# Kernel optimization log

Measured on AMD Instinct MI355X. Metric: run time of the kernel, lower is better.

Reference implementation:

```python
import jax, jax.numpy as jnp
import numpy as np

# ---- constants matching the original module's globals ----
H = 16          # self.h: number of bit levels; self.n = h per the source
TP = 8          # self.tp: parallel coordinate channels
N_K = 2         # random masks per flipped bit
T = 512         # T_train: tokens per block
N_TRNBR = 128   # neighbor count
K_VOCAB = 128   # sampled vocab count
N_VOCAB = 50257 # full vocab size V for sampled softmax correction
D = 256         # embedding dim
RATIO_COS = 1.0
RATIO_CRO = 0.1
C_CNC = 2 * H * N_K + 1  # candidate locations per token = 65


def setup_inputs() -> dict:
    key = jax.random.key(0)
    ks = jax.random.split(key, 8)
    n = H  # code: self.n = h
    sta_loc = jax.random.randint(ks[0], (T, TP), 1 - n, n, dtype=jnp.int32)
    nei_loc = jax.random.randint(ks[1], (T, N_TRNBR, TP), 1 - n, n, dtype=jnp.int32)
    voc_loc = jax.random.randint(ks[2], (T, K_VOCAB, TP), 1 - n, n, dtype=jnp.int32)
    sta_emb = jax.random.normal(ks[3], (T, D), dtype=jnp.float32)
    nei_emb = jax.random.normal(ks[4], (T, N_TRNBR, D), dtype=jnp.float32)
    voc_emb = jax.random.normal(ks[5], (T, K_VOCAB, D), dtype=jnp.float32)
    # raw random numbers for generate_random_masks: randint(0, self.n)
    rand_masks = jax.random.randint(ks[6], (T, H, N_K, TP), 0, n, dtype=jnp.int32)
    # converge mode: mask is all ones (generate_mask with converge=True)
    mask = jnp.ones((T, N_TRNBR), dtype=bool)
    return {"sta_loc": sta_loc, "nei_loc": nei_loc, "voc_loc": voc_loc,
            "sta_emb": sta_emb, "nei_emb": nei_emb, "voc_emb": voc_emb,
            "rand_masks": rand_masks, "mask": mask}


def _cos_similarity(c1, c2):
    # sign product: (+1 if >=0 else -1) for each operand
    sg = ((2 * (c1 >= 0).astype(jnp.int32) - 1) *
          (2 * (c2 >= 0).astype(jnp.int32) - 1)).astype(jnp.float32)
    x = ((jnp.abs(c1) ^ jnp.abs(c2)) + 1).astype(jnp.float32)
    # torch.frexp exponent of v>=1 equals floor(log2(v)) + 1
    expo = jnp.floor(jnp.log2(x)) + 1.0
    return sg * (1.0 - expo / H)


def _connection(sta_loc, rand_masks):
    bits = jnp.arange(H, dtype=jnp.int32)
    flip_masks = (1 << bits)                          # [H]
    flipped = sta_loc[:, None, :] ^ flip_masks[None, :, None]  # [T,H,TP]
    # note operator precedence in source: rn & (2**i - 1)
    rm = rand_masks & (flip_masks - 1)[None, :, None, None]    # [T,H,N_K,TP]
    res = (flipped[:, :, None, :] ^ rm).reshape(sta_loc.shape[0], H * N_K, TP)
    return jnp.concatenate([res, sta_loc[:, None, :], -res], axis=1)  # [T,C,TP]


def _normalize(x):
    return x / jnp.maximum(jnp.linalg.norm(x, axis=-1, keepdims=True), 1e-12)


def reference(sta_loc, nei_loc, voc_loc, sta_emb, nei_emb, voc_emb, rand_masks, mask):
    cnc_loc = _connection(sta_loc, rand_masks)          # [T, C, TP]
    lth = mask.sum(axis=1).astype(jnp.float32) + 1e-12  # [T]

    # euclidean-space cosine targets: [T, N_trnbr]
    eu_cos_val = jnp.einsum('td,tnd->tn', _normalize(sta_emb), _normalize(nei_emb))
    # use_eu_norm == True branch: ||sta|| * ||voc|| -> [T, K_vocab]
    eu_cro_nrm = (jnp.linalg.norm(sta_emb, axis=-1, keepdims=True) *
                  jnp.linalg.norm(voc_emb, axis=-1))

    pos_loc = jnp.concatenate([nei_loc, voc_loc], axis=1)           # [T, P, TP]
    cos_sta_pos = _cos_similarity(sta_loc[:, None, :], pos_loc)     # [T, P, TP]
    cos_sta_pos_sum = cos_sta_pos.sum(axis=-1)                      # [T, P]
    cos_cnc_pos = _cos_similarity(cnc_loc[:, None, :, :], pos_loc[:, :, None, :])  # [T,P,C,TP]
    ct_val = (cos_sta_pos_sum[:, :, None, None]
              - cos_sta_pos[:, :, None, :] + cos_cnc_pos) / TP      # [T,P,C,TP]

    # cosine-matching loss over neighbors
    eu = eu_cos_val[:, :, None, None]                               # [T,N,1,1]
    loss_cos = ((ct_val[:, :N_TRNBR] - eu) ** 2 * jnp.abs(eu)
                * mask[:, :, None, None].astype(jnp.float32))
    loss_cos = loss_cos.sum(axis=1) / lth[:, None, None]            # [T, C, TP]

    # sampled softmax CE (uniform proposal), positive class at vocab index 0
    z = ct_val[:, N_TRNBR:] * eu_cro_nrm[:, :, None, None]          # [T, K, C, TP]
    corr = jnp.where(jnp.arange(K_VOCAB) == 0, 0.0,
                     jnp.log(N_VOCAB / K_VOCAB)).astype(jnp.float32)
    zc = z + corr[None, :, None, None]
    loss_cro = jax.scipy.special.logsumexp(zc, axis=1) - zc[:, 0]   # [T, C, TP]

    loss_tot = RATIO_COS * loss_cos + RATIO_CRO * loss_cro

    # get_best_loc with cur_portion=1.0, cur_tp=tp -> pure argmin selection
    idx = jnp.argmin(loss_tot, axis=1)                              # [T, TP]
    gather = lambda a: jnp.take_along_axis(a, idx[:, None, :], axis=1)[:, 0]
    selected_locs = gather(cnc_loc)                                 # [T, TP]
    real_loss_cos = gather(loss_cos).mean(axis=-1)                  # [T]
    real_loss_cro = gather(loss_cro).mean(axis=-1)
    real_loss_tot = gather(loss_tot).mean(axis=-1)
    return selected_locs, real_loss_cos, real_loss_cro, real_loss_tot
```

## Files before the change

### kernel.cpp

```cpp
#include <hip/hip_runtime.h>
#include <math.h>

#define T_DIM 512
#define TP 8
#define H 16
#define N_K 2
#define N_TRNBR 128
#define K_VOCAB 128
#define D_DIM 256
#define C_CNC 65
#define NPOS 256
#define BLOCK 576

__device__ __forceinline__ float cos_sim(int c1, int c2) {
    float sg = ((c1 >= 0) == (c2 >= 0)) ? 1.0f : -1.0f;
    int a1 = c1 < 0 ? -c1 : c1;
    int a2 = c2 < 0 ? -c2 : c2;
    int x = (a1 ^ a2) + 1;
    int expo = 32 - __clz(x);
    return sg * (1.0f - (float)expo * 0.0625f);
}

__global__ __launch_bounds__(BLOCK) void critigraph_kernel(
    const int* __restrict__ sta_loc,
    const int* __restrict__ nei_loc,
    const int* __restrict__ voc_loc,
    const float* __restrict__ sta_emb,
    const float* __restrict__ nei_emb,
    const float* __restrict__ voc_emb,
    const int* __restrict__ rand_masks,
    float* __restrict__ out)
{
    const int t = blockIdx.x;
    const int tid = threadIdx.x;

    __shared__ int   s_sta[TP];
    __shared__ int   s_rand[H * N_K * TP];
    __shared__ int   s_pos[NPOS * TP];
    __shared__ float s_csp[NPOS * TP];
    __shared__ float s_css[NPOS];
    __shared__ float s_eu[128];
    __shared__ float s_nrm[128];
    __shared__ float s_dot[128], s_nn[128], s_vv[128];
    __shared__ float s_ss;
    __shared__ float s_lcos[C_CNC * TP], s_lcro[C_CNC * TP], s_ltot[C_CNC * TP];
    __shared__ int   s_cnc[C_CNC * TP];
    __shared__ float s_sel[3 * TP];

    if (tid < TP) s_sta[tid] = sta_loc[t * TP + tid];
    if (tid < H * N_K * TP) s_rand[tid] = rand_masks[t * H * N_K * TP + tid];

    if (tid < 512) {
        const int g = tid >> 2, sub = tid & 3;
        const float4* sp = reinterpret_cast<const float4*>(sta_emb + (size_t)t * D_DIM);
        const float4* np_ = reinterpret_cast<const float4*>(nei_emb + ((size_t)t * 128 + g) * D_DIM);
        const float4* vp = reinterpret_cast<const float4*>(voc_emb + ((size_t)t * 128 + g) * D_DIM);
        float sd = 0.f, nn = 0.f, vv = 0.f, ss = 0.f;
        #pragma unroll
        for (int i = 0; i < 16; ++i) {
            const int i4 = sub + 4 * i;
            float4 a = sp[i4];
            float4 b = np_[i4];
            float4 c = vp[i4];
            sd += a.x * b.x + a.y * b.y + a.z * b.z + a.w * b.w;
            nn += b.x * b.x + b.y * b.y + b.z * b.z + b.w * b.w;
            vv += c.x * c.x + c.y * c.y + c.z * c.z + c.w * c.w;
            ss += a.x * a.x + a.y * a.y + a.z * a.z + a.w * a.w;
        }
        sd += __shfl_xor(sd, 1); sd += __shfl_xor(sd, 2);
        nn += __shfl_xor(nn, 1); nn += __shfl_xor(nn, 2);
        vv += __shfl_xor(vv, 1); vv += __shfl_xor(vv, 2);
        ss += __shfl_xor(ss, 1); ss += __shfl_xor(ss, 2);
        if (sub == 0) {
            s_dot[g] = sd; s_nn[g] = nn; s_vv[g] = vv;
            if (g == 0) s_ss = ss;
        }
    }
    __syncthreads();

    if (tid < 128) {
        const float ns = sqrtf(s_ss);
        const float cs = fmaxf(ns, 1e-12f);
        const float cn = fmaxf(sqrtf(s_nn[tid]), 1e-12f);
        s_eu[tid] = s_dot[tid] / (cn * cs);
        s_nrm[tid] = ns * sqrtf(s_vv[tid]);
    }

    for (int item = tid; item < NPOS * TP; item += BLOCK) {
        const int j = item >> 3, p = item & 7;
        const int pl = (j < 128) ? nei_loc[((size_t)t * 128 + j) * TP + p]
                                 : voc_loc[((size_t)t * 128 + (j - 128)) * TP + p];
        s_pos[j * TP + p] = pl;
        s_csp[j * TP + p] = cos_sim(s_sta[p], pl);
    }
    __syncthreads();

    if (tid < NPOS) {
        float s = 0.f;
        #pragma unroll
        for (int p = 0; p < TP; ++p) s += s_csp[tid * TP + p];
        s_css[tid] = s;
    }
    __syncthreads();

    if (tid < C_CNC * TP) {
        const int c = tid >> 3, p = tid & 7;
        const int sta = s_sta[p];
        int v;
        if (c == 32) {
            v = sta;
        } else {
            const int cc = (c < 32) ? c : (c - 33);
            const int h = cc >> 1, k = cc & 1;
            const int r = (sta ^ (1 << h)) ^ (s_rand[(h * N_K + k) * TP + p] & ((1 << h) - 1));
            v = (c < 32) ? r : -r;
        }

        float lc = 0.f;
        for (int j = 0; j < 128; ++j) {
            const float ct = (s_css[j] - s_csp[j * TP + p] + cos_sim(v, s_pos[j * TP + p])) * 0.125f;
            const float e = s_eu[j];
            const float d = ct - e;
            lc += d * d * fabsf(e);
        }
        lc *= (1.0f / 128.0f);

        const float CORR = logf(50257.0f / 128.0f);
        float m = -INFINITY, ssum = 0.f, z0 = 0.f;
        for (int k = 0; k < 128; ++k) {
            const int j = 128 + k;
            const float ct = (s_css[j] - s_csp[j * TP + p] + cos_sim(v, s_pos[j * TP + p])) * 0.125f;
            const float z = ct * s_nrm[k] + ((k == 0) ? 0.0f : CORR);
            if (k == 0) z0 = z;
            const float nm = fmaxf(m, z);
            ssum = ssum * expf(m - nm) + expf(z - nm);
            m = nm;
        }
        const float lcro = m + logf(ssum) - z0;

        s_lcos[c * TP + p] = lc;
        s_lcro[c * TP + p] = lcro;
        s_ltot[c * TP + p] = lc + 0.1f * lcro;
        s_cnc[c * TP + p] = v;
    }
    __syncthreads();

    if (tid < TP) {
        const int p = tid;
        float best = s_ltot[p];
        int bi = 0;
        for (int c = 1; c < C_CNC; ++c) {
            const float vv = s_ltot[c * TP + p];
            if (vv < best) { best = vv; bi = c; }
        }
        out[t * TP + p] = (float)s_cnc[bi * TP + p];
        s_sel[p] = s_lcos[bi * TP + p];
        s_sel[TP + p] = s_lcro[bi * TP + p];
        s_sel[2 * TP + p] = s_ltot[bi * TP + p];
    }
    __syncthreads();

    if (tid == 0) {
        float a = 0.f, b = 0.f, c = 0.f;
        #pragma unroll
        for (int p = 0; p < TP; ++p) {
            a += s_sel[p]; b += s_sel[TP + p]; c += s_sel[2 * TP + p];
        }
        out[T_DIM * TP + t] = a * (1.0f / TP);
        out[T_DIM * TP + T_DIM + t] = b * (1.0f / TP);
        out[T_DIM * TP + 2 * T_DIM + t] = c * (1.0f / TP);
    }
}

extern "C" void kernel_launch(void* const* d_in, const int* in_sizes, int n_in,
                              void* d_out, int out_size, void* d_ws, size_t ws_size,
                              hipStream_t stream) {
    const int* sta_loc = (const int*)d_in[0];
    const int* nei_loc = (const int*)d_in[1];
    const int* voc_loc = (const int*)d_in[2];
    const float* sta_emb = (const float*)d_in[3];
    const float* nei_emb = (const float*)d_in[4];
    const float* voc_emb = (const float*)d_in[5];
    const int* rand_masks = (const int*)d_in[6];
    float* out = (float*)d_out;

    critigraph_kernel<<<T_DIM, BLOCK, 0, stream>>>(
        sta_loc, nei_loc, voc_loc, sta_emb, nei_emb, voc_emb, rand_masks, out);
}
```

Measured before the change: 218.3 us.

## Split per-token work across neighbor/vocab blocks and add finalize kernel

The single fused kernel becomes two. The main kernel uses a 2D grid, so one block handles the neighbor (cosine) side and another the vocab (cross-entropy) side. Each writes per-candidate losses to workspace, and a small second kernel does the argmin and the averaging. It also adds a bit-trick cosine similarity, precomputed per-position partial sums, exp2-based online softmax with a select-only rescale, and wave-parallel handling of the 65th candidate. This removes the serial dependency where each thread did both 128-length loops, and raises parallelism. The cost is a second launch and a round trip of the losses through global memory.

```diff
diff --git a/kernel.cpp b/kernel.cpp
--- a/kernel.cpp
+++ b/kernel.cpp
@@ -3,25 +3,24 @@
 
 #define T_DIM 512
 #define TP 8
-#define H 16
-#define N_K 2
-#define N_TRNBR 128
-#define K_VOCAB 128
-#define D_DIM 256
-#define C_CNC 65
-#define NPOS 256
-#define BLOCK 576
-
-__device__ __forceinline__ float cos_sim(int c1, int c2) {
-    float sg = ((c1 >= 0) == (c2 >= 0)) ? 1.0f : -1.0f;
-    int a1 = c1 < 0 ? -c1 : c1;
-    int a2 = c2 < 0 ? -c2 : c2;
-    int x = (a1 ^ a2) + 1;
-    int expo = 32 - __clz(x);
-    return sg * (1.0f - (float)expo * 0.0625f);
-}
-
-__global__ __launch_bounds__(BLOCK) void critigraph_kernel(
+#define NC 65
+#define NJ 128
+#define LOG2E 1.4426950408889634f
+#define LN2   0.6931471805599453f
+
+__device__ __forceinline__ float csim(int va, int vs, int qmix) {
+    const int sgn = (vs ^ qmix) & 0x80000000;
+    const int x = va ^ (qmix & 0x7fffffff);
+    const float u0 = fmaf((float)__clz(x + 1), 0.0625f, -1.0f);
+    return __int_as_float(__float_as_int(u0) ^ sgn);
+}
+
+__device__ __forceinline__ int make_v(int c, int sta, int rnd_cc_h , int h) {
+    const int r = (sta ^ (1 << h)) ^ (rnd_cc_h & ((1 << h) - 1));
+    return r;
+}
+
+__global__ __launch_bounds__(512, 8) void cg_main(
     const int* __restrict__ sta_loc,
     const int* __restrict__ nei_loc,
     const int* __restrict__ voc_loc,
@@ -29,146 +28,217 @@
     const float* __restrict__ nei_emb,
     const float* __restrict__ voc_emb,
     const int* __restrict__ rand_masks,
+    float* __restrict__ wcos,
+    float* __restrict__ wcro)
+{
+    const int t = blockIdx.x;
+    const int side = blockIdx.y;
+    const int tid = threadIdx.x;
+
+    __shared__ int2  s_pc[NJ * TP];
+    __shared__ float s_w[NJ];
+    __shared__ float s_css[NJ];
+    __shared__ float s_dot[NJ], s_nn[NJ];
+    __shared__ float s_ss;
+    __shared__ int   s_sta[TP];
+    __shared__ int   s_rand[256];
+
+    if (tid < TP) s_sta[tid] = sta_loc[t * TP + tid];
+    if (tid < 256) s_rand[tid] = rand_masks[t * 256 + tid];
+
+    {
+        const float* emb = (side == 0) ? nei_emb : voc_emb;
+        const int g = tid >> 2, sub = tid & 3;
+        const float4* ep = (const float4*)(emb + ((size_t)t * NJ + g) * 256);
+        const float4* sp = (const float4*)(sta_emb + (size_t)t * 256);
+        float dd = 0.f, nn = 0.f, ss = 0.f;
+        #pragma unroll
+        for (int i = 0; i < 16; ++i) {
+            const int i4 = sub + 4 * i;
+            const float4 a = sp[i4];
+            const float4 b = ep[i4];
+            dd += a.x * b.x + a.y * b.y + a.z * b.z + a.w * b.w;
+            nn += b.x * b.x + b.y * b.y + b.z * b.z + b.w * b.w;
+            if (g == 0) ss += a.x * a.x + a.y * a.y + a.z * a.z + a.w * a.w;
+        }
+        dd += __shfl_xor(dd, 1); dd += __shfl_xor(dd, 2);
+        nn += __shfl_xor(nn, 1); nn += __shfl_xor(nn, 2);
+        if (g == 0) { ss += __shfl_xor(ss, 1); ss += __shfl_xor(ss, 2); }
+        if (sub == 0) { s_dot[g] = dd; s_nn[g] = nn; if (g == 0) s_ss = ss; }
+    }
+    __syncthreads();
+
+    {
+        const int* loc = (side == 0) ? nei_loc : voc_loc;
+        #pragma unroll
+        for (int item = tid; item < NJ * TP; item += 512) {
+            const int p = item & 7;
+            const int pl = loc[(size_t)t * (NJ * TP) + item];
+            const int qm = (pl < 0 ? -pl : pl) | (pl & 0x80000000);
+            const int sta = s_sta[p];
+            const float csp = csim(sta < 0 ? -sta : sta, sta & 0x80000000, qm);
+            s_pc[item].x = qm;
+            s_pc[item].y = __float_as_int(csp);
+        }
+    }
+    __syncthreads();
+
+    if (tid < NJ) {
+        float cs = 0.f;
+        #pragma unroll
+        for (int p = 0; p < TP; ++p) cs += __int_as_float(s_pc[tid * TP + p].y);
+        s_css[tid] = cs;
+        const float ns = sqrtf(s_ss);
+        if (side == 0) {
+            s_w[tid] = s_dot[tid] / (fmaxf(sqrtf(s_nn[tid]), 1e-12f) * fmaxf(ns, 1e-12f));
+        } else {
+            s_w[tid] = ns * sqrtf(s_nn[tid]) * (0.125f * LOG2E);
+        }
+    }
+    __syncthreads();
+
+    {
+        const float corrl2 = logf(50257.0f / 128.0f) * LOG2E;
+        #pragma unroll
+        for (int item = tid; item < NJ * TP; item += 512) {
+            const int j = item >> 3;
+            const float csp = __int_as_float(s_pc[item].y);
+            const float b = s_css[j] - csp;
+            float val;
+            if (side == 0) val = b;
+            else val = fmaf(b, s_w[j], (j == 0) ? 0.0f : corrl2);
+            s_pc[item].y = __float_as_int(val);
+        }
+    }
+    __syncthreads();
+
+    {
+        const int c = tid >> 3, p = tid & 7;
+        const int sta = s_sta[p];
+        int v;
+        if (c == 32) v = sta;
+        else {
+            const int cc = (c < 32) ? c : (c - 33);
+            const int h = cc >> 1;
+            const int r = make_v(c, sta, s_rand[cc * TP + p], h);
+            v = (c < 32) ? r : -r;
+        }
+        const int va = v < 0 ? -v : v;
+        const int vs = v & 0x80000000;
+
+        if (side == 0) {
+            float lc = 0.f;
+            #pragma unroll 4
+            for (int j = 0; j < NJ; ++j) {
+                const int2 pc = s_pc[j * TP + p];
+                const float u = csim(va, vs, pc.x);
+                const float e = s_w[j];
+                const float d = fmaf(__int_as_float(pc.y) + u, 0.125f, -e);
+                lc = fmaf(d * d, fabsf(e), lc);
+            }
+            wcos[((size_t)t * NC + c) * TP + p] = lc * 0.0078125f;
+        } else {
+            const int2 pc0 = s_pc[p];
+            const float u0 = csim(va, vs, pc0.x);
+            const float z0 = fmaf(u0, s_w[0], __int_as_float(pc0.y));
+            float m = z0, s = 1.0f;
+            #pragma unroll 4
+            for (int k = 1; k < NJ; ++k) {
+                const int2 pc = s_pc[k * TP + p];
+                const float u = csim(va, vs, pc.x);
+                const float z = fmaf(u, s_w[k], __int_as_float(pc.y));
+                const float nm = fmaxf(m, z);
+                const float e = exp2f(fminf(z, m) - nm);
+                const bool gt = z > m;
+                s = fmaf(s, gt ? e : 1.0f, gt ? 1.0f : e);
+                m = nm;
+            }
+            wcro[((size_t)t * NC + c) * TP + p] = (m - z0 + log2f(s)) * LN2;
+        }
+    }
+
+    {
+        const int p = tid >> 6;
+        const int lane = tid & 63;
+        const int sta = s_sta[p];
+        const int v = -((sta ^ (1 << 15)) ^ (s_rand[31 * TP + p] & 0x7fff));
+        const int va = v < 0 ? -v : v;
+        const int vs = v & 0x80000000;
+
+        if (side == 0) {
+            float lc = 0.f;
+            #pragma unroll
+            for (int jj = 0; jj < 2; ++jj) {
+                const int j = 2 * lane + jj;
+                const int2 pc = s_pc[j * TP + p];
+                const float u = csim(va, vs, pc.x);
+                const float e = s_w[j];
+                const float d = fmaf(__int_as_float(pc.y) + u, 0.125f, -e);
+                lc = fmaf(d * d, fabsf(e), lc);
+            }
+            #pragma unroll
+            for (int off = 1; off < 64; off <<= 1) lc += __shfl_xor(lc, off);
+            if (lane == 0) wcos[((size_t)t * NC + 64) * TP + p] = lc * 0.0078125f;
+        } else {
+            const int ka = 2 * lane, kb = 2 * lane + 1;
+            const int2 pa = s_pc[ka * TP + p];
+            const int2 pb = s_pc[kb * TP + p];
+            const float za = fmaf(csim(va, vs, pa.x), s_w[ka], __int_as_float(pa.y));
+            const float zb = fmaf(csim(va, vs, pb.x), s_w[kb], __int_as_float(pb.y));
+            float m = fmaxf(za, zb);
+            float s = exp2f(za - m) + exp2f(zb - m);
+            const float z0 = za;
+            #pragma unroll
+            for (int off = 1; off < 64; off <<= 1) {
+                const float om = __shfl_xor(m, off);
+                const float os = __shfl_xor(s, off);
+                const float nm = fmaxf(m, om);
+                s = fmaf(s, exp2f(m - nm), os * exp2f(om - nm));
+                m = nm;
+            }
+            if (lane == 0) wcro[((size_t)t * NC + 64) * TP + p] = (m - z0 + log2f(s)) * LN2;
+        }
+    }
+}
+
+__global__ __launch_bounds__(64) void cg_fin(
+    const int* __restrict__ sta_loc, const int* __restrict__ rand_masks,
+    const float* __restrict__ wcos, const float* __restrict__ wcro,
     float* __restrict__ out)
 {
     const int t = blockIdx.x;
     const int tid = threadIdx.x;
-
-    __shared__ int   s_sta[TP];
-    __shared__ int   s_rand[H * N_K * TP];
-    __shared__ int   s_pos[NPOS * TP];
-    __shared__ float s_csp[NPOS * TP];
-    __shared__ float s_css[NPOS];
-    __shared__ float s_eu[128];
-    __shared__ float s_nrm[128];
-    __shared__ float s_dot[128], s_nn[128], s_vv[128];
-    __shared__ float s_ss;
-    __shared__ float s_lcos[C_CNC * TP], s_lcro[C_CNC * TP], s_ltot[C_CNC * TP];
-    __shared__ int   s_cnc[C_CNC * TP];
-    __shared__ float s_sel[3 * TP];
-
-    if (tid < TP) s_sta[tid] = sta_loc[t * TP + tid];
-    if (tid < H * N_K * TP) s_rand[tid] = rand_masks[t * H * N_K * TP + tid];
-
-    if (tid < 512) {
-        const int g = tid >> 2, sub = tid & 3;
-        const float4* sp = reinterpret_cast<const float4*>(sta_emb + (size_t)t * D_DIM);
-        const float4* np_ = reinterpret_cast<const float4*>(nei_emb + ((size_t)t * 128 + g) * D_DIM);
-        const float4* vp = reinterpret_cast<const float4*>(voc_emb + ((size_t)t * 128 + g) * D_DIM);
-        float sd = 0.f, nn = 0.f, vv = 0.f, ss = 0.f;
-        #pragma unroll
-        for (int i = 0; i < 16; ++i) {
-            const int i4 = sub + 4 * i;
-            float4 a = sp[i4];
-            float4 b = np_[i4];
-            float4 c = vp[i4];
-            sd += a.x * b.x + a.y * b.y + a.z * b.z + a.w * b.w;
-            nn += b.x * b.x + b.y * b.y + b.z * b.z + b.w * b.w;
-            vv += c.x * c.x + c.y * c.y + c.z * c.z + c.w * c.w;
-            ss += a.x * a.x + a.y * a.y + a.z * a.z + a.w * a.w;
-        }
-        sd += __shfl_xor(sd, 1); sd += __shfl_xor(sd, 2);
-        nn += __shfl_xor(nn, 1); nn += __shfl_xor(nn, 2);
-        vv += __shfl_xor(vv, 1); vv += __shfl_xor(vv, 2);
-        ss += __shfl_xor(ss, 1); ss += __shfl_xor(ss, 2);
-        if (sub == 0) {
-            s_dot[g] = sd; s_nn[g] = nn; s_vv[g] = vv;
-            if (g == 0) s_ss = ss;
-        }
-    }
-    __syncthreads();
-
-    if (tid < 128) {
-        const float ns = sqrtf(s_ss);
-        const float cs = fmaxf(ns, 1e-12f);
-        const float cn = fmaxf(sqrtf(s_nn[tid]), 1e-12f);
-        s_eu[tid] = s_dot[tid] / (cn * cs);
-        s_nrm[tid] = ns * sqrtf(s_vv[tid]);
-    }
-
-    for (int item = tid; item < NPOS * TP; item += BLOCK) {
-        const int j = item >> 3, p = item & 7;
-        const int pl = (j < 128) ? nei_loc[((size_t)t * 128 + j) * TP + p]
-                                 : voc_loc[((size_t)t * 128 + (j - 128)) * TP + p];
-        s_pos[j * TP + p] = pl;
-        s_csp[j * TP + p] = cos_sim(s_sta[p], pl);
-    }
-    __syncthreads();
-
-    if (tid < NPOS) {
-        float s = 0.f;
-        #pragma unroll
-        for (int p = 0; p < TP; ++p) s += s_csp[tid * TP + p];
-        s_css[tid] = s;
-    }
-    __syncthreads();
-
-    if (tid < C_CNC * TP) {
-        const int c = tid >> 3, p = tid & 7;
-        const int sta = s_sta[p];
+    float sc = 0.f, sr = 0.f, st = 0.f;
+    if (tid < TP) {
+        const float* pc = wcos + (size_t)t * NC * TP + tid;
+        const float* pr = wcro + (size_t)t * NC * TP + tid;
+        float best = INFINITY, blc = 0.f, blr = 0.f;
+        int bc = 0;
+        for (int c = 0; c < NC; ++c) {
+            const float lc = pc[c * TP];
+            const float lr = pr[c * TP];
+            const float lt = fmaf(0.1f, lr, lc);
+            if (lt < best) { best = lt; bc = c; blc = lc; blr = lr; }
+        }
+        const int sta = sta_loc[t * TP + tid];
         int v;
-        if (c == 32) {
-            v = sta;
-        } else {
-            const int cc = (c < 32) ? c : (c - 33);
-            const int h = cc >> 1, k = cc & 1;
-            const int r = (sta ^ (1 << h)) ^ (s_rand[(h * N_K + k) * TP + p] & ((1 << h) - 1));
-            v = (c < 32) ? r : -r;
-        }
-
-        float lc = 0.f;
-        for (int j = 0; j < 128; ++j) {
-            const float ct = (s_css[j] - s_csp[j * TP + p] + cos_sim(v, s_pos[j * TP + p])) * 0.125f;
-            const float e = s_eu[j];
-            const float d = ct - e;
-            lc += d * d * fabsf(e);
-        }
-        lc *= (1.0f / 128.0f);
-
-        const float CORR = logf(50257.0f / 128.0f);
-        float m = -INFINITY, ssum = 0.f, z0 = 0.f;
-        for (int k = 0; k < 128; ++k) {
-            const int j = 128 + k;
-            const float ct = (s_css[j] - s_csp[j * TP + p] + cos_sim(v, s_pos[j * TP + p])) * 0.125f;
-            const float z = ct * s_nrm[k] + ((k == 0) ? 0.0f : CORR);
-            if (k == 0) z0 = z;
-            const float nm = fmaxf(m, z);
-            ssum = ssum * expf(m - nm) + expf(z - nm);
-            m = nm;
-        }
-        const float lcro = m + logf(ssum) - z0;
-
-        s_lcos[c * TP + p] = lc;
-        s_lcro[c * TP + p] = lcro;
-        s_ltot[c * TP + p] = lc + 0.1f * lcro;
-        s_cnc[c * TP + p] = v;
-    }
-    __syncthreads();
-
-    if (tid < TP) {
-        const int p = tid;
-        float best = s_ltot[p];
-        int bi = 0;
-        for (int c = 1; c < C_CNC; ++c) {
-            const float vv = s_ltot[c * TP + p];
-            if (vv < best) { best = vv; bi = c; }
-        }
-        out[t * TP + p] = (float)s_cnc[bi * TP + p];
-        s_sel[p] = s_lcos[bi * TP + p];
-        s_sel[TP + p] = s_lcro[bi * TP + p];
-        s_sel[2 * TP + p] = s_ltot[bi * TP + p];
-    }
-    __syncthreads();
-
+        if (bc == 32) v = sta;
+        else {
+            const int cc = (bc < 32) ? bc : (bc - 33);
+            const int h = cc >> 1;
+            const int r = (sta ^ (1 << h)) ^ (rand_masks[t * 256 + cc * TP + tid] & ((1 << h) - 1));
+            v = (bc < 32) ? r : -r;
+        }
+        out[t * TP + tid] = (float)v;
+        sc = blc; sr = blr; st = best;
+    }
+    sc += __shfl_xor(sc, 1); sc += __shfl_xor(sc, 2); sc += __shfl_xor(sc, 4);
+    sr += __shfl_xor(sr, 1); sr += __shfl_xor(sr, 2); sr += __shfl_xor(sr, 4);
+    st += __shfl_xor(st, 1); st += __shfl_xor(st, 2); st += __shfl_xor(st, 4);
     if (tid == 0) {
-        float a = 0.f, b = 0.f, c = 0.f;
-        #pragma unroll
-        for (int p = 0; p < TP; ++p) {
-            a += s_sel[p]; b += s_sel[TP + p]; c += s_sel[2 * TP + p];
-        }
-        out[T_DIM * TP + t] = a * (1.0f / TP);
-        out[T_DIM * TP + T_DIM + t] = b * (1.0f / TP);
-        out[T_DIM * TP + 2 * T_DIM + t] = c * (1.0f / TP);
+        out[T_DIM * TP + t] = sc * 0.125f;
+        out[T_DIM * TP + T_DIM + t] = sr * 0.125f;
+        out[T_DIM * TP + 2 * T_DIM + t] = st * 0.125f;
     }
 }
 
@@ -184,6 +254,10 @@
     const int* rand_masks = (const int*)d_in[6];
     float* out = (float*)d_out;
 
-    critigraph_kernel<<<T_DIM, BLOCK, 0, stream>>>(
-        sta_loc, nei_loc, voc_loc, sta_emb, nei_emb, voc_emb, rand_masks, out);
-}
+    float* wcos = (float*)d_ws;
+    float* wcro = wcos + (size_t)T_DIM * NC * TP;
+
+    cg_main<<<dim3(T_DIM, 2), 512, 0, stream>>>(
+        sta_loc, nei_loc, voc_loc, sta_emb, nei_emb, voc_emb, rand_masks, wcos, wcro);
+    cg_fin<<<T_DIM, 64, 0, stream>>>(sta_loc, rand_masks, wcos, wcro, out);
+}
```

New measurement: 218.2 us. No clear change (-0.1%).
